# Optimization experiments

Measured on AMD Instinct MI355X. Metric: run time of the kernel, lower is better.

The kernel has to match this reference:

```python
import jax, jax.numpy as jnp
import numpy as np

N_HEAD = 12
EPS = 1e-6


def setup_inputs() -> dict:
    key = jax.random.key(0)
    k1, k2, k3 = jax.random.split(key, 3)
    B, T, C = 2, 2048, 768
    x = jax.random.normal(k1, (B, T, C), dtype=jnp.float32)
    c_attn_w = jax.random.normal(k2, (3 * C, C), dtype=jnp.float32) * 0.02
    c_proj_w = jax.random.normal(k3, (C, C), dtype=jnp.float32) * 0.02
    temperature = jnp.ones((1,), dtype=jnp.float32) * np.sqrt(C // N_HEAD)
    return {"x": x, "c_attn_w": c_attn_w, "c_proj_w": c_proj_w, "temperature": temperature}


def reference(x, c_attn_w, c_proj_w, temperature):
    B, T, C = x.shape
    H = N_HEAD
    D = C // H
    qkv = x @ c_attn_w.T  # [B,T,3C] (no bias)
    q, k, v = jnp.split(qkv, 3, axis=2)
    # [B,H,T,D]
    q = q.reshape(B, T, H, D).transpose(0, 2, 1, 3)
    k = k.reshape(B, T, H, D).transpose(0, 2, 1, 3)
    v = v.reshape(B, T, H, D).transpose(0, 2, 1, 3)

    # autocorrelation via FFT along time axis, zero-padded to 2T
    fft_len = 2 * T
    q_fft = jnp.fft.rfft(q, n=fft_len, axis=2)
    k_fft = jnp.fft.rfft(k, n=fft_len, axis=2)
    corr = jnp.fft.irfft(q_fft * jnp.conj(k_fft), n=fft_len, axis=2)[:, :, :T, :]
    corr_weights = corr.mean(axis=-1) / (temperature + EPS)  # [B,H,T] over lag

    # causal lag mask: position t may use lags 0..t
    t_idx = jnp.arange(T)
    lag_mask = t_idx[None, :] <= t_idx[:, None]  # [T(pos), T(lag)]
    weights_masked = jnp.where(lag_mask[None, None], corr_weights[:, :, None, :], -jnp.inf)
    attn = jax.nn.softmax(weights_masked, axis=-1)  # [B,H,T,T] over lags
    attn = jnp.nan_to_num(attn)

    # Original gathers v at source position s = clamp(t - lag, 0), producing a
    # (B,H,T,T,D) tensor. Since lags > t have zero weight, this is exactly
    # y[t] = sum_{s<=t} attn[t, t-s] * v[s]. Build the position-score matrix by
    # gathering attn along the lag axis — avoids the 5D blowup, same math.
    lag_idx = jnp.clip(t_idx[:, None] - t_idx[None, :], 0)  # [T(pos), T(src)]
    scores = jnp.take_along_axis(attn, lag_idx[None, None], axis=-1)
    scores = jnp.where(lag_mask[None, None], scores, 0.0)  # zero out s > t
    y = jnp.einsum('bhts,bhsd->bhtd', scores, v)

    y = y.transpose(0, 2, 1, 3).reshape(B, T, C)
    return y @ c_proj_w.T
```

## Files before the change

kernel.cpp:

```cpp
#include <hip/hip_runtime.h>

#define T_ 2048
#define B_ 2
#define H_ 12
#define C_ 768
#define M_ 4096
#define BH_ (B_ * H_)
#define RSTR 2200

typedef __attribute__((ext_vector_type(4))) float f32x4;
typedef __attribute__((ext_vector_type(16))) float f32x16;
typedef __attribute__((ext_vector_type(8))) __bf16 bf16x8;
typedef __attribute__((ext_vector_type(4))) __bf16 bf16x4;

#define GLOAD16(GP, LP)                                                   \
  __builtin_amdgcn_global_load_lds(                                       \
      (__attribute__((address_space(1))) void*)(GP),                      \
      (__attribute__((address_space(3))) void*)(LP), 16, 0, 0)


__global__ __launch_bounds__(256) void cvt3_k(const float* __restrict__ x,
                                              const float* __restrict__ ca,
                                              const float* __restrict__ cp,
                                              __bf16* __restrict__ xb,
                                              __bf16* __restrict__ wb,
                                              __bf16* __restrict__ pb) {
  const int id = blockIdx.x;
  const float* src;
  __bf16* dst;
  size_t base;
  if (id < 1536) { src = x; dst = xb; base = (size_t)id * 2048; }
  else if (id < 2400) { src = ca; dst = wb; base = (size_t)(id - 1536) * 2048; }
  else { src = cp; dst = pb; base = (size_t)(id - 2400) * 2048; }
  const size_t o = base + (size_t)threadIdx.x * 8;
  f32x4 v0 = *(const f32x4*)(src + o);
  f32x4 v1 = *(const f32x4*)(src + o + 4);
  bf16x8 r;
#pragma unroll
  for (int j = 0; j < 4; ++j) { r[j] = (__bf16)v0[j]; r[4 + j] = (__bf16)v1[j]; }
  *(bf16x8*)(dst + o) = r;
}

__global__ __launch_bounds__(256) void gemm_qkv(const __bf16* __restrict__ A,
                                                const __bf16* __restrict__ Bm,
                                                __bf16* __restrict__ Qp,
                                                __bf16* __restrict__ Kp,
                                                __bf16* __restrict__ Vp) {
  __shared__ __align__(16) __bf16 sA[4096];
  __shared__ __align__(16) __bf16 sB[4096];
  const int tid = threadIdx.x;
  const int id = blockIdx.x;
  const int lg = (id & 7) * 72 + (id >> 3);
  const int m0 = (lg / 18) * 128, n0 = (lg % 18) * 128;
  const bool isV = (n0 >= 1536);
  const int lane = tid & 63, w = tid >> 6;
  const int wr = w >> 1, wc = w & 1;
  const int fr = lane & 15;
  const int ko = (lane >> 4) << 3;
  const int srow = lane >> 2, scol = (lane & 3) << 3;
  const __bf16* Ab = A + (size_t)(m0 + srow) * 768 + scol;
  const __bf16* Bb = Bm + (size_t)(n0 + srow) * 768 + scol;
  const int c0 = 2 * w, c1 = 2 * w + 1;
  f32x4 acc[4][4] = {};

  if (isV) {
    for (int k0 = 0; k0 < 768; k0 += 32) {
      GLOAD16(Ab + (size_t)c0 * 16 * 768 + k0, &sA[c0 * 512]);
      GLOAD16(Ab + (size_t)c1 * 16 * 768 + k0, &sA[c1 * 512]);
      GLOAD16(Bb + (size_t)c0 * 16 * 768 + k0, &sB[c0 * 512]);
      GLOAD16(Bb + (size_t)c1 * 16 * 768 + k0, &sB[c1 * 512]);
      __syncthreads();
      bf16x8 a[4], b[4];
#pragma unroll
      for (int m = 0; m < 4; ++m) a[m] = *(const bf16x8*)&sA[(wr * 64 + m * 16 + fr) * 32 + ko];
#pragma unroll
      for (int n = 0; n < 4; ++n) b[n] = *(const bf16x8*)&sB[(wc * 64 + n * 16 + fr) * 32 + ko];
#pragma unroll
      for (int m = 0; m < 4; ++m)
#pragma unroll
        for (int n = 0; n < 4; ++n)
          acc[m][n] = __builtin_amdgcn_mfma_f32_16x16x32_bf16(a[m], b[n], acc[m][n], 0, 0, 0);
      __syncthreads();
    }
    const int orow = (lane >> 4) << 2, ocol = lane & 15;
#pragma unroll
    for (int m = 0; m < 4; ++m)
#pragma unroll
      for (int n = 0; n < 4; ++n) {
        int r = m0 + wr * 64 + m * 16 + orow;
        int c = n0 + wc * 64 + n * 16 + ocol;
        int hd = c - 1536;
        int h = hd >> 6, d = hd & 63;
        int b = r >> 11, t = r & 2047;
        int bh = b * H_ + h;
        int chunk = t >> 6, sk = t & 63;
        int kc = sk >> 4, hf = (sk >> 3) & 1, j0 = sk & 7;
        bf16x4 pk;
#pragma unroll
        for (int j = 0; j < 4; ++j) pk[j] = (__bf16)acc[m][n][j];
        *(bf16x4*)(Vp + ((size_t)bh * 32 + chunk) * 4096 + (d >> 5) * 2048 +
                   kc * 512 + (hf * 32 + (d & 31)) * 8 + j0) = pk;
      }
  } else {
    for (int k0 = 0; k0 < 768; k0 += 32) {
      GLOAD16(Ab + (size_t)c0 * 16 * 768 + k0, &sA[c0 * 512]);
      GLOAD16(Ab + (size_t)c1 * 16 * 768 + k0, &sA[c1 * 512]);
      GLOAD16(Bb + (size_t)c0 * 16 * 768 + k0, &sB[c0 * 512]);
      GLOAD16(Bb + (size_t)c1 * 16 * 768 + k0, &sB[c1 * 512]);
      __syncthreads();
      bf16x8 a[4], b[4];
#pragma unroll
      for (int m = 0; m < 4; ++m) a[m] = *(const bf16x8*)&sA[(wr * 64 + m * 16 + fr) * 32 + ko];
#pragma unroll
      for (int n = 0; n < 4; ++n) b[n] = *(const bf16x8*)&sB[(wc * 64 + n * 16 + fr) * 32 + ko];
#pragma unroll
      for (int m = 0; m < 4; ++m)
#pragma unroll
        for (int n = 0; n < 4; ++n)
          acc[m][n] = __builtin_amdgcn_mfma_f32_16x16x32_bf16(b[n], a[m], acc[m][n], 0, 0, 0);
      __syncthreads();
    }
    const int tcol = lane & 15, dbase = (lane >> 4) << 2;
#pragma unroll
    for (int m = 0; m < 4; ++m)
#pragma unroll
      for (int n = 0; n < 4; ++n) {
        int t4 = m0 + wr * 64 + m * 16 + tcol;
        int c = n0 + wc * 64 + n * 16 + dbase;
        int sec = c / 768;
        int hd = c - sec * 768;
        int h = hd >> 6, d = hd & 63;
        int b = t4 >> 11, t = t4 & 2047;
        int bh = b * H_ + h;
        int tile = t >> 5, rr = t & 31;
        int kc = d >> 4, half = (d >> 3) & 1, dj = d & 7;
        bf16x4 pk;
#pragma unroll
        for (int j = 0; j < 4; ++j) pk[j] = (__bf16)acc[m][n][j];
        *(bf16x4*)((sec == 0 ? Qp : Kp) + ((size_t)bh * 64 + tile) * 2048 +
                   kc * 512 + (half * 32 + rr) * 8 + dj) = pk;
      }
  }
}

__global__ __launch_bounds__(256) void gemm_out(const __bf16* __restrict__ A,
                                                const __bf16* __restrict__ Bm,
                                                float* __restrict__ C) {
  __shared__ __align__(16) __bf16 sA[2048];
  __shared__ __align__(16) __bf16 sB[2048];
  const int tid = threadIdx.x;
  const int id = blockIdx.x;
  const int lg = (id & 7) * 96 + (id >> 3);
  const int m0 = (lg / 12) * 64, n0 = (lg % 12) * 64;
  const int lane = tid & 63, w = tid >> 6;
  const int wr = w >> 1, wc = w & 1;
  const int fr = lane & 15;
  const int ko = (lane >> 4) << 3;
  const int srow = tid >> 2, scol = (tid & 3) << 3;
  const __bf16* Ab = A + (size_t)(m0 + srow) * 768 + scol;
  const __bf16* Bb = Bm + (size_t)(n0 + srow) * 768 + scol;
  f32x4 acc[2][2] = {};
  for (int k0 = 0; k0 < 768; k0 += 32) {
    GLOAD16(Ab + k0, &sA[w * 512]);
    GLOAD16(Bb + k0, &sB[w * 512]);
    __syncthreads();
    bf16x8 a[2], b[2];
#pragma unroll
    for (int m = 0; m < 2; ++m) a[m] = *(const bf16x8*)&sA[(wr * 32 + m * 16 + fr) * 32 + ko];
#pragma unroll
    for (int n = 0; n < 2; ++n) b[n] = *(const bf16x8*)&sB[(wc * 32 + n * 16 + fr) * 32 + ko];
#pragma unroll
    for (int m = 0; m < 2; ++m)
#pragma unroll
      for (int n = 0; n < 2; ++n)
        acc[m][n] = __builtin_amdgcn_mfma_f32_16x16x32_bf16(a[m], b[n], acc[m][n], 0, 0, 0);
    __syncthreads();
  }
  const int orow = (lane >> 4) << 2, ocol = lane & 15;
#pragma unroll
  for (int m = 0; m < 2; ++m)
#pragma unroll
    for (int n = 0; n < 2; ++n) {
      int r = m0 + wr * 32 + m * 16 + orow;
      int c = n0 + wc * 32 + n * 16 + ocol;
#pragma unroll
      for (int j = 0; j < 4; ++j) C[(size_t)(r + j) * 768 + c] = acc[m][n][j];
    }
}

__global__ __launch_bounds__(256) void corr_k3(const __bf16* __restrict__ Qp,
                                               const __bf16* __restrict__ Kp,
                                               float* __restrict__ P36) {
  __shared__ __align__(16) char smem[40960];
  __bf16* sQ = (__bf16*)smem;
  __bf16* sK = (__bf16*)(smem + 4096);
  const int tid = threadIdx.x;
  int id = blockIdx.x;
  int sub = id >> 3;
  const int bh = (id & 7) * 3 + sub / 36;
  const int pi = sub % 36;
  int x = pi, qb = 0;
  while (x >= 8 - qb) { x -= 8 - qb; ++qb; }
  const int tc = qb + x;
  const int lane = tid & 63, w = tid >> 6;

  const __bf16* qbase = Qp + ((size_t)bh << 17);
  const __bf16* kbase = Kp + ((size_t)bh << 17);
  const int wq = w << 9;

  const int smin = 8 * (tc - qb) - 8;
#pragma unroll
  for (int li = 0; li < 8; ++li) {
    int si = smin + li;
    if (si >= 0) GLOAD16(kbase + (size_t)si * 2048 + tid * 8, sK + li * 2048 + wq);
  }

  int r0 = 8 - 2 * w;
  int r1 = 7 - 2 * w;
  int ss = 8;
  const int qA = 8 * qb + 2 * w;
  f32x16 acc0 = {}, acc1 = {};

  for (int tau = 0; tau < 8; ++tau) {
    const int ti = 8 * tc + tau;
    GLOAD16(qbase + (size_t)ti * 2048 + tid * 8, sQ + wq);
    GLOAD16(kbase + (size_t)(ti - 8 * qb) * 2048 + tid * 8, sK + ss * 2048 + wq);
    __syncthreads();
    bf16x8 qv[4];
    const __bf16* qf = sQ + lane * 8;
#pragma unroll
    for (int kc = 0; kc < 4; ++kc) qv[kc] = *(const bf16x8*)(qf + kc * 512);
    const int si0 = ti - qA;
    if (si0 >= 0) {
      const __bf16* kf = sK + r0 * 2048 + lane * 8;
#pragma unroll
      for (int kc = 0; kc < 4; ++kc)
        acc0 = __builtin_amdgcn_mfma_f32_32x32x16_bf16(qv[kc], *(const bf16x8*)(kf + kc * 512), acc0, 0, 0, 0);
    }
    if (si0 - 1 >= 0) {
      const __bf16* kf = sK + r1 * 2048 + lane * 8;
#pragma unroll
      for (int kc = 0; kc < 4; ++kc)
        acc1 = __builtin_amdgcn_mfma_f32_32x32x16_bf16(qv[kc], *(const bf16x8*)(kf + kc * 512), acc1, 0, 0, 0);
    }
    __syncthreads();
    if (++r0 == 9) r0 = 0;
    if (++r1 == 9) r1 = 0;
    if (++ss == 9) ss = 0;
  }

  float* tile = (float*)smem;
  float* prow = (float*)(smem + 16896);
  for (int i = tid; i < 1152; i += 256) prow[i] = 0.f;
  const int col = lane & 31, hi = lane >> 5;
  const int d = lane - 31;
#pragma unroll
  for (int b01 = 0; b01 < 2; ++b01) {
    const f32x16* ac = (b01 == 0) ? &acc0 : &acc1;
#pragma unroll
    for (int j = 0; j < 16; ++j) {
      int row = (j & 3) + ((j >> 2) << 3) + 4 * hi;
      tile[w * 1056 + row * 33 + col] = (*ac)[j];
    }
    __syncthreads();
    if (lane < 63) {
      float s = 0.f;
#pragma unroll
      for (int c = 0; c < 32; ++c) {
        int r = c + d;
        bool ok = (unsigned)r < 32u;
        float val = tile[w * 1056 + (ok ? r : 0) * 33 + c];
        s += ok ? val : 0.f;
      }
      prow[w * 288 + 32 * (2 * w + b01) + d + 32] += s;
    }
    __syncthreads();
  }

  float* Pd = P36 + ((size_t)pi * BH_ + bh) * T_;
  float ov[8];
#pragma unroll
  for (int u = 0; u < 8; ++u) {
    int L = (tid << 3) + u;
    int l = L - 256 * qb;
    float s = 0.f;
    if (l >= -31 && l < 256)
      s = prow[l + 32] + prow[288 + l + 32] + prow[576 + l + 32] + prow[864 + l + 32];
    ov[u] = s;
  }
  *(f32x4*)(Pd + (tid << 3)) = *(f32x4*)&ov[0];
  *(f32x4*)(Pd + (tid << 3) + 4) = *(f32x4*)&ov[4];
}

__global__ __launch_bounds__(256) void soft_k(const float* __restrict__ P,
                                              const float* __restrict__ temp,
                                              __bf16* __restrict__ Rb,
                                              float* __restrict__ zinv) {
  __shared__ float se[T_];
  __shared__ float lm[4], wsum[4];
  const int bh = blockIdx.x, tid = threadIdx.x;
  const int lane = tid & 63, wid = tid >> 6;
  const float scale = 1.0f / (64.0f * (temp[0] + 1e-6f));
  f32x4 sa = {}, sb = {};
#pragma unroll
  for (int j = 0; j < 36; ++j) {
    const float* pp = P + ((size_t)j * BH_ + bh) * T_ + (tid << 3);
    sa += *(const f32x4*)pp;
    sb += *(const f32x4*)(pp + 4);
  }
  float v[8];
#pragma unroll
  for (int i = 0; i < 4; ++i) { v[i] = sa[i] * scale; v[4 + i] = sb[i] * scale; }
  float m = v[0];
#pragma unroll
  for (int i = 1; i < 8; ++i) m = fmaxf(m, v[i]);
#pragma unroll
  for (int off = 1; off < 64; off <<= 1) m = fmaxf(m, __shfl_xor(m, off));
  if (lane == 0) lm[wid] = m;
  __syncthreads();
  m = fmaxf(fmaxf(lm[0], lm[1]), fmaxf(lm[2], lm[3]));
  float ex[8], pr[8], run = 0;
#pragma unroll
  for (int i = 0; i < 8; ++i) { ex[i] = __expf(v[i] - m); run += ex[i]; pr[i] = run; }
  float s = run;
  for (int off = 1; off < 64; off <<= 1) {
    float o = __shfl_up(s, off);
    if (lane >= off) s += o;
  }
  if (lane == 63) wsum[wid] = s;
  __syncthreads();
  float base = s - run;
  for (int jw = 0; jw < wid; ++jw) base += wsum[jw];
#pragma unroll
  for (int i = 0; i < 8; ++i) {
    int t = (tid << 3) + i;
    zinv[(size_t)bh * T_ + t] = 1.0f / (base + pr[i]);
    se[t] = ex[i];
  }
  __syncthreads();
  __bf16* rb = Rb + (size_t)bh * 8 * RSTR;
  for (int c = tid; c < RSTR / 8; c += 256) {
    int i0 = c << 3;
#pragma unroll
    for (int p = 0; p < 8; ++p) {
      bf16x8 ovv;
#pragma unroll
      for (int e = 0; e < 8; ++e) {
        int idx = T_ - 1 - p - (i0 + e);
        ovv[e] = (__bf16)((idx >= 0) ? se[idx] : 0.f);
      }
      *(bf16x8*)(rb + p * RSTR + i0) = ovv;
    }
  }
}

__global__ __launch_bounds__(256) void conv_k(const __bf16* __restrict__ Vp,
                                              const __bf16* __restrict__ Rb,
                                              const float* __restrict__ zinv,
                                              __bf16* __restrict__ y2b) {
  __shared__ __align__(16) __bf16 revc[8 * RSTR];
  const int tid = threadIdx.x;
  int id = blockIdx.x;
  int sub = id >> 3;
  const int bh = (id & 7) * 3 + (sub >> 4);
  const int pr = sub & 15;
  const int lane = tid & 63, w = tid >> 6;

  const __bf16* rb = Rb + (size_t)bh * 8 * RSTR;
  for (int c = tid; c < RSTR; c += 256)
    *(bf16x8*)&revc[c << 3] = *(const bf16x8*)(rb + ((size_t)c << 3));
  __syncthreads();

  const int fr = lane & 31, kg = (lane >> 5) << 3;
  const int tt = (w < 2) ? (64 * pr + 32 * w) : (64 * (31 - pr) + 32 * (w - 2));
  const int trow = tt + fr;
  const int pp = (T_ - 1 - trow) & 7;
  const int obase = (T_ - 1 - trow) - pp;
  const __bf16* vpb = Vp + (size_t)bh * 131072 + (lane << 3);
  f32x16 acc0 = {}, acc1 = {};
  const int nst = (tt >> 6) + 1;

  bf16x8 A00, A01, A02, A03, A10, A11, A12, A13;
  bf16x8 B00, B01, B02, B03, B10, B11, B12, B13;
  bf16x8 C00, C01, C02, C03, C10, C11, C12, C13;

#define LOADV(P, CH)                                                          \
  {                                                                           \
    const __bf16* vb_ = vpb + (size_t)(CH) * 4096;                            \
    P##00 = *(const bf16x8*)(vb_);          P##01 = *(const bf16x8*)(vb_ + 512);  \
    P##02 = *(const bf16x8*)(vb_ + 1024);   P##03 = *(const bf16x8*)(vb_ + 1536); \
    P##10 = *(const bf16x8*)(vb_ + 2048);   P##11 = *(const bf16x8*)(vb_ + 2560); \
    P##12 = *(const bf16x8*)(vb_ + 3072);   P##13 = *(const bf16x8*)(vb_ + 3584); \
  }
#define MSTEP(P, ST)                                                          \
  {                                                                           \
    const int ab_ = pp * RSTR + obase + (ST) * 64 + kg;                       \
    bf16x8 a0_ = *(const bf16x8*)&revc[ab_];                                  \
    bf16x8 a1_ = *(const bf16x8*)&revc[ab_ + 16];                             \
    bf16x8 a2_ = *(const bf16x8*)&revc[ab_ + 32];                             \
    bf16x8 a3_ = *(const bf16x8*)&revc[ab_ + 48];                             \
    acc0 = __builtin_amdgcn_mfma_f32_32x32x16_bf16(a0_, P##00, acc0, 0, 0, 0);\
    acc1 = __builtin_amdgcn_mfma_f32_32x32x16_bf16(a0_, P##10, acc1, 0, 0, 0);\
    acc0 = __builtin_amdgcn_mfma_f32_32x32x16_bf16(a1_, P##01, acc0, 0, 0, 0);\
    acc1 = __builtin_amdgcn_mfma_f32_32x32x16_bf16(a1_, P##11, acc1, 0, 0, 0);\
    acc0 = __builtin_amdgcn_mfma_f32_32x32x16_bf16(a2_, P##02, acc0, 0, 0, 0);\
    acc1 = __builtin_amdgcn_mfma_f32_32x32x16_bf16(a2_, P##12, acc1, 0, 0, 0);\
    acc0 = __builtin_amdgcn_mfma_f32_32x32x16_bf16(a3_, P##03, acc0, 0, 0, 0);\
    acc1 = __builtin_amdgcn_mfma_f32_32x32x16_bf16(a3_, P##13, acc1, 0, 0, 0);\
  }

  LOADV(A, 0);
  if (nst > 1) LOADV(B, 1);
  if (nst > 2) LOADV(C, 2);
  int st = 0;
  while (true) {
    MSTEP(A, st); if (st + 3 < nst) LOADV(A, st + 3); if (++st >= nst) break;
    MSTEP(B, st); if (st + 3 < nst) LOADV(B, st + 3); if (++st >= nst) break;
    MSTEP(C, st); if (st + 3 < nst) LOADV(C, st + 3); if (++st >= nst) break;
  }
#undef LOADV
#undef MSTEP

  const int b = bh / H_, h = bh % H_;
  const int ocol = lane & 31, rbj = (lane >> 5) << 2;
  const float* zp = zinv + (size_t)bh * T_;
#pragma unroll
  for (int j = 0; j < 16; ++j) {
    int row = (j & 3) + ((j >> 2) << 3) + rbj;
    int t = tt + row;
    float zi = zp[t];
    __bf16* yr = y2b + ((size_t)b * T_ + t) * C_ + h * 64;
    yr[ocol] = (__bf16)(acc0[j] * zi);
    yr[32 + ocol] = (__bf16)(acc1[j] * zi);
  }
}

extern "C" void kernel_launch(void* const* d_in, const int* in_sizes, int n_in,
                              void* d_out, int out_size, void* d_ws, size_t ws_size,
                              hipStream_t stream) {
  const float* x = (const float*)d_in[0];
  const float* c_attn = (const float*)d_in[1];
  const float* c_proj = (const float*)d_in[2];
  const float* temp = (const float*)d_in[3];
  float* out = (float*)d_out;

  __bf16* Qp = (__bf16*)d_ws;
  __bf16* Kp = Qp + (size_t)3145728;
  __bf16* Vp = Kp + (size_t)3145728;
  __bf16* Rb = Vp + (size_t)3145728;
  float* zinv = (float*)(Rb + 422400);
  float* P36 = zinv + 49152;
  __bf16* pb = (__bf16*)(P36 + 1769472);
  __bf16* xb = pb + 589824;
  __bf16* wb = xb + 3145728;
  __bf16* y2b = xb;

  cvt3_k<<<dim3(2688), 256, 0, stream>>>(x, c_attn, c_proj, xb, wb, pb);
  gemm_qkv<<<dim3(576), 256, 0, stream>>>(xb, wb, Qp, Kp, Vp);
  corr_k3<<<dim3(864), 256, 0, stream>>>(Qp, Kp, P36);
  soft_k<<<dim3(BH_), 256, 0, stream>>>(P36, temp, Rb, zinv);
  conv_k<<<dim3(384), 256, 0, stream>>>(Vp, Rb, zinv, y2b);
  gemm_out<<<dim3(768), 256, 0, stream>>>(y2b, pb, out);
}
```

Baseline: 91.37 us.

## Split conv_k reduction across two wave groups with LDS partial-sum combine

Doubles the conv_k block size to 512 threads. The second group of four waves handles the second half of the causal reduction steps for the same output tiles, and the two halves are summed through shared memory before the scaled bf16 store. The aim is more waves per block to hide load latency and to shorten the serial MFMA chain, which matters most for the long tiles near the end of the sequence. In exchange it adds 32KB of LDS, a __syncthreads, and duplicate register pressure, which could lower occupancy.

```diff
diff --git a/kernel.cpp b/kernel.cpp
--- a/kernel.cpp
+++ b/kernel.cpp
@@ -354,31 +354,36 @@
   }
 }
 
-__global__ __launch_bounds__(256) void conv_k(const __bf16* __restrict__ Vp,
+__global__ __launch_bounds__(512) void conv_k(const __bf16* __restrict__ Vp,
                                               const __bf16* __restrict__ Rb,
                                               const float* __restrict__ zinv,
                                               __bf16* __restrict__ y2b) {
   __shared__ __align__(16) __bf16 revc[8 * RSTR];
+  __shared__ __align__(16) float part[4][2][1024];
   const int tid = threadIdx.x;
   int id = blockIdx.x;
   int sub = id >> 3;
   const int bh = (id & 7) * 3 + (sub >> 4);
   const int pr = sub & 15;
   const int lane = tid & 63, w = tid >> 6;
+  const int w4 = w & 3, shalf = w >> 2;
 
   const __bf16* rb = Rb + (size_t)bh * 8 * RSTR;
-  for (int c = tid; c < RSTR; c += 256)
+  for (int c = tid; c < RSTR; c += 512)
     *(bf16x8*)&revc[c << 3] = *(const bf16x8*)(rb + ((size_t)c << 3));
   __syncthreads();
 
   const int fr = lane & 31, kg = (lane >> 5) << 3;
-  const int tt = (w < 2) ? (64 * pr + 32 * w) : (64 * (31 - pr) + 32 * (w - 2));
+  const int tt = (w4 < 2) ? (64 * pr + 32 * w4) : (64 * (31 - pr) + 32 * (w4 - 2));
   const int trow = tt + fr;
   const int pp = (T_ - 1 - trow) & 7;
   const int obase = (T_ - 1 - trow) - pp;
   const __bf16* vpb = Vp + (size_t)bh * 131072 + (lane << 3);
   f32x16 acc0 = {}, acc1 = {};
   const int nst = (tt >> 6) + 1;
+  const int nst0 = (nst + 1) >> 1;
+  const int sbgn = shalf ? nst0 : 0;
+  const int send = shalf ? nst : nst0;
 
   bf16x8 A00, A01, A02, A03, A10, A11, A12, A13;
   bf16x8 B00, B01, B02, B03, B10, B11, B12, B13;
@@ -409,29 +414,46 @@
     acc1 = __builtin_amdgcn_mfma_f32_32x32x16_bf16(a3_, P##13, acc1, 0, 0, 0);\
   }
 
-  LOADV(A, 0);
-  if (nst > 1) LOADV(B, 1);
-  if (nst > 2) LOADV(C, 2);
-  int st = 0;
-  while (true) {
-    MSTEP(A, st); if (st + 3 < nst) LOADV(A, st + 3); if (++st >= nst) break;
-    MSTEP(B, st); if (st + 3 < nst) LOADV(B, st + 3); if (++st >= nst) break;
-    MSTEP(C, st); if (st + 3 < nst) LOADV(C, st + 3); if (++st >= nst) break;
+  if (sbgn < send) {
+    LOADV(A, sbgn);
+    if (sbgn + 1 < send) LOADV(B, sbgn + 1);
+    if (sbgn + 2 < send) LOADV(C, sbgn + 2);
+    int st = sbgn;
+    while (true) {
+      MSTEP(A, st); if (st + 3 < send) LOADV(A, st + 3); if (++st >= send) break;
+      MSTEP(B, st); if (st + 3 < send) LOADV(B, st + 3); if (++st >= send) break;
+      MSTEP(C, st); if (st + 3 < send) LOADV(C, st + 3); if (++st >= send) break;
+    }
   }
 #undef LOADV
 #undef MSTEP
 
-  const int b = bh / H_, h = bh % H_;
-  const int ocol = lane & 31, rbj = (lane >> 5) << 2;
-  const float* zp = zinv + (size_t)bh * T_;
-#pragma unroll
-  for (int j = 0; j < 16; ++j) {
-    int row = (j & 3) + ((j >> 2) << 3) + rbj;
-    int t = tt + row;
-    float zi = zp[t];
-    __bf16* yr = y2b + ((size_t)b * T_ + t) * C_ + h * 64;
-    yr[ocol] = (__bf16)(acc0[j] * zi);
-    yr[32 + ocol] = (__bf16)(acc1[j] * zi);
+  if (shalf) {
+#pragma unroll
+    for (int j = 0; j < 16; ++j) {
+      part[w4][0][j * 64 + lane] = acc0[j];
+      part[w4][1][j * 64 + lane] = acc1[j];
+    }
+  }
+  __syncthreads();
+  if (!shalf) {
+#pragma unroll
+    for (int j = 0; j < 16; ++j) {
+      acc0[j] += part[w4][0][j * 64 + lane];
+      acc1[j] += part[w4][1][j * 64 + lane];
+    }
+    const int b = bh / H_, h = bh % H_;
+    const int ocol = lane & 31, rbj = (lane >> 5) << 2;
+    const float* zp = zinv + (size_t)bh * T_;
+#pragma unroll
+    for (int j = 0; j < 16; ++j) {
+      int row = (j & 3) + ((j >> 2) << 3) + rbj;
+      int t = tt + row;
+      float zi = zp[t];
+      __bf16* yr = y2b + ((size_t)b * T_ + t) * C_ + h * 64;
+      yr[ocol] = (__bf16)(acc0[j] * zi);
+      yr[32 + ocol] = (__bf16)(acc1[j] * zi);
+    }
   }
 }
 
@@ -459,6 +481,6 @@
   gemm_qkv<<<dim3(576), 256, 0, stream>>>(xb, wb, Qp, Kp, Vp);
   corr_k3<<<dim3(864), 256, 0, stream>>>(Qp, Kp, P36);
   soft_k<<<dim3(BH_), 256, 0, stream>>>(P36, temp, Rb, zinv);
-  conv_k<<<dim3(384), 256, 0, stream>>>(Vp, Rb, zinv, y2b);
+  conv_k<<<dim3(384), 512, 0, stream>>>(Vp, Rb, zinv, y2b);
   gemm_out<<<dim3(768), 256, 0, stream>>>(y2b, pb, out);
 }
```

Result: no change. 93.14 us (+1.9%).
